# Kernel optimization log

Hardware: AMD Instinct MI355X
Metric: run time of the kernel (lower is better)

Reference implementation:

```python
import jax, jax.numpy as jnp
import numpy as np

N_QUBITS = 8
DEPTH = 2
INPUT_DIM = 64
HIDDEN_DIM = 8
SEQ_LEN = 128
BATCH = 512
DIM = 2 ** N_QUBITS


def _build_perm():
    """Compose the depth*n CNOT ring (CNOT(i,(i+1)%n) for i in range(n), repeated DEPTH times)
    into a single basis-state permutation. Wire 0 is the most-significant qubit (torchquantum order).
    CNOT is an involution on basis states: new[s] = old[f(s)], f flips target bit iff control bit set.
    Sequential composition: perm <- perm[f_j]."""
    n = N_QUBITS
    perm = np.arange(DIM)
    for _ in range(DEPTH):
        for c in range(n):
            t = (c + 1) % n
            s = np.arange(DIM)
            cbit = (s >> (n - 1 - c)) & 1
            fs = np.where(cbit == 1, s ^ (1 << (n - 1 - t)), s)
            perm = perm[fs]
    return jnp.asarray(perm, dtype=jnp.int32)


def _build_signs():
    s = np.arange(DIM)[:, None]
    w = np.arange(N_QUBITS)[None, :]
    bits = (s >> (N_QUBITS - 1 - w)) & 1
    return jnp.asarray(1.0 - 2.0 * bits, dtype=jnp.float32)  # [DIM, n]


PERM = _build_perm()
SIGNS = _build_signs()


def _qlayer(ang):
    """QLayer: RX(ang_i) on wire i of |0...0> (encoder RX + trainable RX fused since RX(a)RX(b)=RX(a+b)),
    then DEPTH CNOT-ring layers (precomputed permutation), then PauliZ expectation per wire.
    ang: [B, n] -> returns [B, n]."""
    half = 0.5 * ang
    v0 = jnp.cos(half).astype(jnp.complex64)          # [B, n]
    v1 = (-1j) * jnp.sin(half).astype(jnp.complex64)  # RX|0> = cos(t/2)|0> - i sin(t/2)|1>
    vecs = jnp.stack([v0, v1], axis=-1)               # [B, n, 2]
    b = ang.shape[0]
    state = jnp.ones((b, 1), jnp.complex64)
    for w in range(N_QUBITS):  # build product state, wire 0 most significant
        state = (state[:, :, None] * vecs[:, w, None, :]).reshape(b, -1)
    state = state[:, PERM]  # apply composed CNOT entanglers
    probs = jnp.real(state * jnp.conj(state)).astype(jnp.float32)  # [B, 2^n]
    return probs @ SIGNS  # [B, n] PauliZ expectations


def setup_inputs() -> dict:
    key = jax.random.key(0)
    ks = jax.random.split(key, 14)
    d = {"inputs": jax.random.normal(ks[0], (SEQ_LEN, BATCH, INPUT_DIM), jnp.float32)}
    fan_in = INPUT_DIM + HIDDEN_DIM
    scale = 1.0 / np.sqrt(fan_in)
    names = ["f", "i", "u", "o"]
    for j, nm in enumerate(names):
        d[f"W_{nm}"] = jax.random.uniform(ks[1 + 3 * j], (N_QUBITS, fan_in), jnp.float32, -scale, scale)
        d[f"b_{nm}"] = jax.random.uniform(ks[2 + 3 * j], (N_QUBITS,), jnp.float32, -scale, scale)
        d[f"th_{nm}"] = jax.random.normal(ks[3 + 3 * j], (N_QUBITS,), jnp.float32) * 0.1
    return d


def reference(inputs, W_f, b_f, W_i, b_i, W_u, b_u, W_o, b_o, th_f, th_i, th_u, th_o):
    batch = inputs.shape[1]

    def step(carry, x):
        hx, cx = carry
        comb = jnp.concatenate([x, hx], axis=1)  # [B, input+hidden]
        f = jax.nn.sigmoid(_qlayer(comb @ W_f.T + b_f + th_f))
        i = jax.nn.sigmoid(_qlayer(comb @ W_i.T + b_i + th_i))
        g = jnp.tanh(_qlayer(comb @ W_u.T + b_u + th_u))
        o = jax.nn.sigmoid(_qlayer(comb @ W_o.T + b_o + th_o))
        cx = f * cx + i * g
        hx = o * jnp.tanh(cx)
        return (hx, cx), hx

    init = (jnp.zeros((batch, HIDDEN_DIM), jnp.float32), jnp.zeros((batch, HIDDEN_DIM), jnp.float32))
    (hx, cx), outputs = jax.lax.scan(step, init, inputs)
    return (outputs, (hx, cx))
```

## Files before the change

### kernel.cpp

```cpp
#include <hip/hip_runtime.h>
#include <cstdint>
#include <cstddef>


constexpr int SEQ    = 128;
constexpr int NBATCH = 512;
constexpr int INDIM  = 64;
constexpr int FANIN  = 72;
constexpr long OUT_HX = (long)SEQ * NBATCH * 8;
constexpr long OUT_CX = OUT_HX + (long)NBATCH * 8;

#define SWZ(v, imm) __int_as_float(__builtin_amdgcn_ds_swizzle(__float_as_int(v), (imm)))

__device__ __forceinline__ float fast_cos(float ang) {
    const float rev = ang * 0.15915494309189535f;
    return __builtin_amdgcn_cosf(__builtin_amdgcn_fractf(rev));
}

template <int CTRL> __device__ __forceinline__ float DPPF(float x) {
    return __int_as_float(__builtin_amdgcn_update_dpp(
        0, __float_as_int(x), CTRL, 0xF, 0xF, false));
}
__device__ __forceinline__ float xlane1(float x) { return DPPF<0xB1>(x); }
__device__ __forceinline__ float xlane2(float x) { return DPPF<0x4E>(x); }
__device__ __forceinline__ float xlane4(float x) { return DPPF<0x141>(DPPF<0x1B>(x)); }
__device__ __forceinline__ float xlane8(float x) { return DPPF<0x128>(x); }

__global__ __launch_bounds__(256) void xproj_kernel(
    const float* __restrict__ x,
    const float* __restrict__ Wf, const float* __restrict__ bf, const float* __restrict__ thf,
    const float* __restrict__ Wi, const float* __restrict__ bi, const float* __restrict__ thi,
    const float* __restrict__ Wu, const float* __restrict__ bu, const float* __restrict__ thu,
    const float* __restrict__ Wo, const float* __restrict__ bo, const float* __restrict__ tho,
    float* __restrict__ xp)
{
    __shared__ float lx[128 * 68];
    __shared__ float lbias[32];
    const int tid = threadIdx.x;
    const long rowBase = (long)blockIdx.x * 128;

    if (tid < 32) {
        const int g = tid >> 3, w = tid & 7;
        const float* bg = (g == 0) ? bf : (g == 1) ? bi : (g == 2) ? bu : bo;
        const float* tg = (g == 0) ? thf : (g == 1) ? thi : (g == 2) ? thu : tho;
        lbias[tid] = bg[w] + tg[w];
    }

    const float4* xin = reinterpret_cast<const float4*>(x + rowBase * INDIM);
#pragma unroll
    for (int i = 0; i < 8; ++i) {
        const int f   = i * 256 + tid;
        const int row = f >> 4;
        const int kq  = f & 15;
        *reinterpret_cast<float4*>(&lx[row * 68 + kq * 4]) = xin[f];
    }
    __syncthreads();

    const int og = tid & 3;
    const int q  = tid >> 2;
    const float* Wg = (og == 0) ? Wf : (og == 1) ? Wi : (og == 2) ? Wu : Wo;

    float acc[2][8];
#pragma unroll
    for (int r = 0; r < 2; ++r)
#pragma unroll
        for (int j = 0; j < 8; ++j) acc[r][j] = 0.f;

#pragma unroll
    for (int k4 = 0; k4 < 16; ++k4) {
        const float4 x0 = *reinterpret_cast<const float4*>(&lx[q * 68 + k4 * 4]);
        const float4 x1 = *reinterpret_cast<const float4*>(&lx[(q + 64) * 68 + k4 * 4]);
#pragma unroll
        for (int j = 0; j < 8; ++j) {
            const float4 wv = *reinterpret_cast<const float4*>(Wg + j * FANIN + k4 * 4);
            acc[0][j] = fmaf(x0.x, wv.x, acc[0][j]);
            acc[0][j] = fmaf(x0.y, wv.y, acc[0][j]);
            acc[0][j] = fmaf(x0.z, wv.z, acc[0][j]);
            acc[0][j] = fmaf(x0.w, wv.w, acc[0][j]);
            acc[1][j] = fmaf(x1.x, wv.x, acc[1][j]);
            acc[1][j] = fmaf(x1.y, wv.y, acc[1][j]);
            acc[1][j] = fmaf(x1.z, wv.z, acc[1][j]);
            acc[1][j] = fmaf(x1.w, wv.w, acc[1][j]);
        }
    }

#pragma unroll
    for (int r = 0; r < 2; ++r) {
        float4 o0, o1;
        o0.x = acc[r][0] + lbias[og * 8 + 0];
        o0.y = acc[r][1] + lbias[og * 8 + 1];
        o0.z = acc[r][2] + lbias[og * 8 + 2];
        o0.w = acc[r][3] + lbias[og * 8 + 3];
        o1.x = acc[r][4] + lbias[og * 8 + 4];
        o1.y = acc[r][5] + lbias[og * 8 + 5];
        o1.z = acc[r][6] + lbias[og * 8 + 6];
        o1.w = acc[r][7] + lbias[og * 8 + 7];
        float* dst = xp + (rowBase + q + 64 * r) * 32 + og * 8;
        reinterpret_cast<float4*>(dst)[0] = o0;
        reinterpret_cast<float4*>(dst)[1] = o1;
    }
}

__global__ __launch_bounds__(256) void qlstm_scan_kernel(
    const float* __restrict__ xp,
    const float* __restrict__ Wf, const float* __restrict__ Wi,
    const float* __restrict__ Wu, const float* __restrict__ Wo,
    float* __restrict__ out)
{
    const int tid  = threadIdx.x;
    const int lane = tid & 31;
    const int row  = (blockIdx.x << 3) + (tid >> 5);
    const int g    = (lane & 1) | ((lane >> 3) & 2);
    const int w    = (lane >> 1) & 7;

    const float* Wg = (g == 0) ? Wf : (g == 1) ? Wi : (g == 2) ? Wu : Wo;

    float whx[8];
#pragma unroll
    for (int d = 0; d < 8; ++d) whx[d] = Wg[w * FANIN + 64 + (w ^ d)];

    const unsigned mask = (unsigned)((0x55AAD5EAF5FAFDABull >> (w * 8)) & 0xFFull);
    bool pm[8];
#pragma unroll
    for (int d = 0; d < 8; ++d) pm[d] = ((mask >> (w ^ d)) & 1u) != 0u;

    const bool  isU  = (g == 2);
    const float ZL   = isU ? -2.0f : -1.0f;
    const float A    = isU ?  2.0f :  1.0f;
    const float B    = isU ? -1.0f :  0.0f;
    const bool  gOdd = (lane & 1) != 0;
    const bool  gHi  = (lane & 16) != 0;

    const int col = g * 8 + w;

    float hh0=0.f,hh1=0.f,hh2=0.f,hh3=0.f,hh4=0.f,hh5=0.f,hh6=0.f,hh7=0.f;
    float cxl = 0.f;

    float xv0 = xp[(long)row * 32 + col];
    float xv1 = xp[((long)NBATCH + row) * 32 + col];

    for (int t = 0; t < SEQ; ++t) {
        float xv2 = 0.f;
        if (t + 2 < SEQ) xv2 = xp[((long)(t + 2) * NBATCH + row) * 32 + col];

        const float d0 = fmaf(hh0, whx[0], fmaf(hh1, whx[1], fmaf(hh2, whx[2], hh3 * whx[3])));
        const float d1 = fmaf(hh4, whx[4], fmaf(hh5, whx[5], fmaf(hh6, whx[6], hh7 * whx[7])));
        const float ang = xv0 + d0 + d1;

        const float c = fast_cos(ang);

        const float cc0 = c;
        const float cc1 = xlane2(cc0);
        const float cc2 = xlane4(cc0);
        const float cc3 = xlane4(cc1);
        const float cc4 = xlane8(cc0);
        const float cc5 = xlane8(cc1);
        const float cc6 = xlane8(cc2);
        const float cc7 = xlane8(cc3);

        const float p0 = pm[0] ? cc0 : 1.0f;
        const float p1 = pm[1] ? cc1 : 1.0f;
        const float p2 = pm[2] ? cc2 : 1.0f;
        const float p3 = pm[3] ? cc3 : 1.0f;
        const float p4 = pm[4] ? cc4 : 1.0f;
        const float p5 = pm[5] ? cc5 : 1.0f;
        const float p6 = pm[6] ? cc6 : 1.0f;
        const float p7 = pm[7] ? cc7 : 1.0f;
        const float z = ((p0 * p1) * (p2 * p3)) * ((p4 * p5) * (p6 * p7));

        const float e   = __expf(z * ZL);
        const float act = fmaf(A, __builtin_amdgcn_rcpf(1.0f + e), B);

        const float a01 = xlane1(act);
        const float ae  = gOdd ? a01 : act;
        const float ao  = gOdd ? act : a01;
        const float be  = SWZ(ae, 0x401F);
        const float bo  = SWZ(ao, 0x401F);
        const float fg  = gHi ? be : ae;
        const float ig  = gHi ? bo : ao;
        const float ug  = gHi ? ae : be;
        const float og  = gHi ? ao : bo;

        const float ncx = fmaf(fg, cxl, ig * ug);
        const float et  = __expf(-2.0f * ncx);
        const float tc  = fmaf(2.0f, __builtin_amdgcn_rcpf(1.0f + et), -1.0f);
        const float nhx = og * tc;
        cxl = ncx;

        if ((lane & 0x11) == 0) out[((long)t * NBATCH + row) * 8 + w] = nhx;

        hh0 = nhx;
        hh1 = xlane2(hh0);
        hh2 = xlane4(hh0);
        hh3 = xlane4(hh1);
        hh4 = xlane8(hh0);
        hh5 = xlane8(hh1);
        hh6 = xlane8(hh2);
        hh7 = xlane8(hh3);

        xv0 = xv1; xv1 = xv2;
    }

    if ((lane & 0x11) == 0) {
        out[OUT_HX + (long)row * 8 + w] = hh0;
        out[OUT_CX + (long)row * 8 + w] = cxl;
    }
}

__global__ __launch_bounds__(256) void qlstm_scan_fused(
    const float* __restrict__ x,
    const float* __restrict__ Wf, const float* __restrict__ bf, const float* __restrict__ thf,
    const float* __restrict__ Wi, const float* __restrict__ bi, const float* __restrict__ thi,
    const float* __restrict__ Wu, const float* __restrict__ bu, const float* __restrict__ thu,
    const float* __restrict__ Wo, const float* __restrict__ bo, const float* __restrict__ tho,
    float* __restrict__ out)
{
    const int tid  = threadIdx.x;
    const int lane = tid & 31;
    const int row  = (blockIdx.x << 3) + (tid >> 5);
    const int g    = lane >> 3;
    const int w    = lane & 7;

    const float* Wg = (g == 0) ? Wf : (g == 1) ? Wi : (g == 2) ? Wu : Wo;
    const float* bg = (g == 0) ? bf : (g == 1) ? bi : (g == 2) ? bu : bo;
    const float* tg = (g == 0) ? thf : (g == 1) ? thi : (g == 2) ? thu : tho;

    float wh0, wh1, wh2, wh3, wh4, wh5, wh6, wh7;
    {
        const float4* p = reinterpret_cast<const float4*>(Wg + w * FANIN + 64);
        const float4 a = p[0], b4 = p[1];
        wh0 = a.x; wh1 = a.y; wh2 = a.z; wh3 = a.w;
        wh4 = b4.x; wh5 = b4.y; wh6 = b4.z; wh7 = b4.w;
    }
    const float bias = bg[w] + tg[w];
    float wx[64];
#pragma unroll
    for (int k4 = 0; k4 < 16; ++k4) {
        const float4 v = reinterpret_cast<const float4*>(Wg + w * FANIN)[k4];
        wx[4*k4+0] = v.x; wx[4*k4+1] = v.y; wx[4*k4+2] = v.z; wx[4*k4+3] = v.w;
    }

    const unsigned mask = (unsigned)((0x55AAD5EAF5FAFDABull >> (w * 8)) & 0xFFull);
    const bool  isU = (g == 2);
    const float ZL  = isU ? -2.0f : -1.0f;
    const float A   = isU ?  2.0f :  1.0f;
    const float B   = isU ? -1.0f :  0.0f;

    float h0=0,h1=0,h2=0,h3=0,h4=0,h5=0,h6=0,h7=0, cxl=0, nhx=0;

    for (int t = 0; t < SEQ; ++t) {
        const float4* xr4 = reinterpret_cast<const float4*>(x + ((long)t * NBATCH + row) * INDIM);
        float acc = bias;
#pragma unroll
        for (int k4 = 0; k4 < 16; ++k4) {
            const float4 v = xr4[k4];
            acc = fmaf(v.x, wx[4*k4+0], acc);
            acc = fmaf(v.y, wx[4*k4+1], acc);
            acc = fmaf(v.z, wx[4*k4+2], acc);
            acc = fmaf(v.w, wx[4*k4+3], acc);
        }
        float ang = acc;
        ang += fmaf(h0, wh0, fmaf(h1, wh1, fmaf(h2, wh2, h3 * wh3)))
             + fmaf(h4, wh4, fmaf(h5, wh5, fmaf(h6, wh6, h7 * wh7)));

        const float c = fast_cos(ang);
        const float cb0 = SWZ(c, 0x018); const float cb1 = SWZ(c, 0x038);
        const float cb2 = SWZ(c, 0x058); const float cb3 = SWZ(c, 0x078);
        const float cb4 = SWZ(c, 0x098); const float cb5 = SWZ(c, 0x0B8);
        const float cb6 = SWZ(c, 0x0D8); const float cb7 = SWZ(c, 0x0F8);

        const float p0 = (mask & 0x01u) ? cb0 : 1.0f;
        const float p1 = (mask & 0x02u) ? cb1 : 1.0f;
        const float p2 = (mask & 0x04u) ? cb2 : 1.0f;
        const float p3 = (mask & 0x08u) ? cb3 : 1.0f;
        const float p4 = (mask & 0x10u) ? cb4 : 1.0f;
        const float p5 = (mask & 0x20u) ? cb5 : 1.0f;
        const float p6 = (mask & 0x40u) ? cb6 : 1.0f;
        const float p7 = (mask & 0x80u) ? cb7 : 1.0f;
        const float z = ((p0*p1)*(p2*p3)) * ((p4*p5)*(p6*p7));

        const float e   = __expf(z * ZL);
        const float act = fmaf(A, __builtin_amdgcn_rcpf(1.0f + e), B);

        const float fg = SWZ(act, 0x007);
        const float ig = SWZ(act, 0x107);
        const float ug = SWZ(act, 0x207);
        const float og = SWZ(act, 0x307);

        const float ncx = fmaf(fg, cxl, ig * ug);
        const float et  = __expf(-2.0f * ncx);
        const float tc  = fmaf(2.0f, __builtin_amdgcn_rcpf(1.0f + et), -1.0f);
        nhx = og * tc;
        cxl = ncx;

        if (lane < 8) out[((long)t * NBATCH + row) * 8 + lane] = nhx;

        h0 = SWZ(nhx, 0x000); h1 = SWZ(nhx, 0x020);
        h2 = SWZ(nhx, 0x040); h3 = SWZ(nhx, 0x060);
        h4 = SWZ(nhx, 0x080); h5 = SWZ(nhx, 0x0A0);
        h6 = SWZ(nhx, 0x0C0); h7 = SWZ(nhx, 0x0E0);
    }

    if (lane < 8) {
        out[OUT_HX + (long)row * 8 + lane] = nhx;
        out[OUT_CX + (long)row * 8 + lane] = cxl;
    }
}

extern "C" void kernel_launch(void* const* d_in, const int* in_sizes, int n_in,
                              void* d_out, int out_size, void* d_ws, size_t ws_size,
                              hipStream_t stream)
{
    const float* x = (const float*)d_in[0];

    const float *Wf, *bf, *thf, *Wi, *bi, *thi, *Wu, *bu, *thu, *Wo, *bo, *tho;
    if (in_sizes[3] == 8) {
        Wf = (const float*)d_in[1];  bf = (const float*)d_in[2];  thf = (const float*)d_in[3];
        Wi = (const float*)d_in[4];  bi = (const float*)d_in[5];  thi = (const float*)d_in[6];
        Wu = (const float*)d_in[7];  bu = (const float*)d_in[8];  thu = (const float*)d_in[9];
        Wo = (const float*)d_in[10]; bo = (const float*)d_in[11]; tho = (const float*)d_in[12];
    } else {
        Wf = (const float*)d_in[1];  bf = (const float*)d_in[2];
        Wi = (const float*)d_in[3];  bi = (const float*)d_in[4];
        Wu = (const float*)d_in[5];  bu = (const float*)d_in[6];
        Wo = (const float*)d_in[7];  bo = (const float*)d_in[8];
        thf = (const float*)d_in[9]; thi = (const float*)d_in[10];
        thu = (const float*)d_in[11]; tho = (const float*)d_in[12];
    }

    float* out = (float*)d_out;
    float* xp  = (float*)d_ws;
    const size_t need = (size_t)SEQ * NBATCH * 32 * sizeof(float);

    if (ws_size >= need) {
        xproj_kernel<<<(SEQ * NBATCH) / 128, 256, 0, stream>>>(
            x, Wf, bf, thf, Wi, bi, thi, Wu, bu, thu, Wo, bo, tho, xp);
        qlstm_scan_kernel<<<NBATCH / 8, 256, 0, stream>>>(
            xp, Wf, Wi, Wu, Wo, out);
    } else {
        qlstm_scan_fused<<<NBATCH / 8, 256, 0, stream>>>(
            x, Wf, bf, thf, Wi, bi, thi, Wu, bu, thu, Wo, bo, tho, out);
    }
}
```

Measured before the change: 163.7 us.

## Remap scan lanes to wave64 with permlane32 swap and chunked xp prefetch

Changes the scan kernel's lane layout to use full 64-lane waves with two batch rows per wave. Gate pairs are split across the two 32-lane halves and exchanged with permlane32_swap instead of ds_swizzle. The cross-lane broadcasts are rebuilt with new DPP row controls, and the xp loads are prefetched in 16-step register chunks so the serial dependency chain avoids per-step load latency. The cost is higher register pressure, and the new DPP patterns have to reproduce the old lane mapping exactly for correctness.

```diff
diff --git a/kernel.cpp b/kernel.cpp
--- a/kernel.cpp
+++ b/kernel.cpp
@@ -21,10 +21,18 @@
     return __int_as_float(__builtin_amdgcn_update_dpp(
         0, __float_as_int(x), CTRL, 0xF, 0xF, false));
 }
-__device__ __forceinline__ float xlane1(float x) { return DPPF<0xB1>(x); }
-__device__ __forceinline__ float xlane2(float x) { return DPPF<0x4E>(x); }
-__device__ __forceinline__ float xlane4(float x) { return DPPF<0x141>(DPPF<0x1B>(x)); }
-__device__ __forceinline__ float xlane8(float x) { return DPPF<0x128>(x); }
+
+__device__ __forceinline__ float xlane32(float x, bool hiHalf) {
+#if __has_builtin(__builtin_amdgcn_permlane32_swap)
+    typedef unsigned uint2v __attribute__((ext_vector_type(2)));
+    uint2v r = __builtin_amdgcn_permlane32_swap(
+        __float_as_uint(x), __float_as_uint(x), false, false);
+    return __uint_as_float(hiHalf ? r[0] : r[1]);
+#else
+    (void)hiHalf;
+    return __shfl_xor(x, 32, 64);
+#endif
+}
 
 __global__ __launch_bounds__(256) void xproj_kernel(
     const float* __restrict__ x,
@@ -108,10 +116,13 @@
     float* __restrict__ out)
 {
     const int tid  = threadIdx.x;
-    const int lane = tid & 31;
-    const int row  = (blockIdx.x << 3) + (tid >> 5);
-    const int g    = (lane & 1) | ((lane >> 3) & 2);
+    const int lane = tid & 63;
+    const int wv   = tid >> 6;
+    const int g1   = (lane >> 5) & 1;
+    const int g    = (lane & 1) | (g1 << 1);
     const int w    = (lane >> 1) & 7;
+    const int rsub = (lane >> 4) & 1;
+    const int row  = (blockIdx.x << 3) + (wv << 1) + rsub;
 
     const float* Wg = (g == 0) ? Wf : (g == 1) ? Wi : (g == 2) ? Wu : Wo;
 
@@ -124,84 +135,85 @@
 #pragma unroll
     for (int d = 0; d < 8; ++d) pm[d] = ((mask >> (w ^ d)) & 1u) != 0u;
 
-    const bool  isU  = (g == 2);
-    const float ZL   = isU ? -2.0f : -1.0f;
-    const float A    = isU ?  2.0f :  1.0f;
-    const float B    = isU ? -1.0f :  0.0f;
-    const bool  gOdd = (lane & 1) != 0;
-    const bool  gHi  = (lane & 16) != 0;
+    const bool  isU   = (g == 2);
+    const float ZL    = isU ? -2.0f : -1.0f;
+    const float A     = isU ?  2.0f :  1.0f;
+    const float B     = isU ? -1.0f :  0.0f;
+    const bool  gOdd  = (lane & 1) != 0;
+    const bool  gHi   = g1 != 0;
+    const bool  doOut = (lane & 0x21) == 0;
 
     const int col = g * 8 + w;
 
     float hh0=0.f,hh1=0.f,hh2=0.f,hh3=0.f,hh4=0.f,hh5=0.f,hh6=0.f,hh7=0.f;
     float cxl = 0.f;
 
-    float xv0 = xp[(long)row * 32 + col];
-    float xv1 = xp[((long)NBATCH + row) * 32 + col];
-
-    for (int t = 0; t < SEQ; ++t) {
-        float xv2 = 0.f;
-        if (t + 2 < SEQ) xv2 = xp[((long)(t + 2) * NBATCH + row) * 32 + col];
-
-        const float d0 = fmaf(hh0, whx[0], fmaf(hh1, whx[1], fmaf(hh2, whx[2], hh3 * whx[3])));
-        const float d1 = fmaf(hh4, whx[4], fmaf(hh5, whx[5], fmaf(hh6, whx[6], hh7 * whx[7])));
-        const float ang = xv0 + d0 + d1;
-
-        const float c = fast_cos(ang);
-
-        const float cc0 = c;
-        const float cc1 = xlane2(cc0);
-        const float cc2 = xlane4(cc0);
-        const float cc3 = xlane4(cc1);
-        const float cc4 = xlane8(cc0);
-        const float cc5 = xlane8(cc1);
-        const float cc6 = xlane8(cc2);
-        const float cc7 = xlane8(cc3);
-
-        const float p0 = pm[0] ? cc0 : 1.0f;
-        const float p1 = pm[1] ? cc1 : 1.0f;
-        const float p2 = pm[2] ? cc2 : 1.0f;
-        const float p3 = pm[3] ? cc3 : 1.0f;
-        const float p4 = pm[4] ? cc4 : 1.0f;
-        const float p5 = pm[5] ? cc5 : 1.0f;
-        const float p6 = pm[6] ? cc6 : 1.0f;
-        const float p7 = pm[7] ? cc7 : 1.0f;
-        const float z = ((p0 * p1) * (p2 * p3)) * ((p4 * p5) * (p6 * p7));
-
-        const float e   = __expf(z * ZL);
-        const float act = fmaf(A, __builtin_amdgcn_rcpf(1.0f + e), B);
-
-        const float a01 = xlane1(act);
-        const float ae  = gOdd ? a01 : act;
-        const float ao  = gOdd ? act : a01;
-        const float be  = SWZ(ae, 0x401F);
-        const float bo  = SWZ(ao, 0x401F);
-        const float fg  = gHi ? be : ae;
-        const float ig  = gHi ? bo : ao;
-        const float ug  = gHi ? ae : be;
-        const float og  = gHi ? ao : bo;
-
-        const float ncx = fmaf(fg, cxl, ig * ug);
-        const float et  = __expf(-2.0f * ncx);
-        const float tc  = fmaf(2.0f, __builtin_amdgcn_rcpf(1.0f + et), -1.0f);
-        const float nhx = og * tc;
-        cxl = ncx;
-
-        if ((lane & 0x11) == 0) out[((long)t * NBATCH + row) * 8 + w] = nhx;
-
-        hh0 = nhx;
-        hh1 = xlane2(hh0);
-        hh2 = xlane4(hh0);
-        hh3 = xlane4(hh1);
-        hh4 = xlane8(hh0);
-        hh5 = xlane8(hh1);
-        hh6 = xlane8(hh2);
-        hh7 = xlane8(hh3);
-
-        xv0 = xv1; xv1 = xv2;
-    }
-
-    if ((lane & 0x11) == 0) {
+#define QSTEP(XV, T) do {                                                      \
+    const float d0_ = fmaf(hh0, whx[0], fmaf(hh1, whx[1], fmaf(hh2, whx[2], hh3 * whx[3]))); \
+    const float d1_ = fmaf(hh4, whx[4], fmaf(hh5, whx[5], fmaf(hh6, whx[6], hh7 * whx[7]))); \
+    const float ang_ = (XV) + d0_ + d1_;                                       \
+    const float c0_ = fast_cos(ang_);                                          \
+    const float c1_ = DPPF<0x4E>(c0_);                                         \
+    const float c2_ = DPPF<0x141>(DPPF<0x1B>(c0_));                            \
+    const float c3_ = DPPF<0x141>(DPPF<0xB1>(c0_));                            \
+    const float c4_ = DPPF<0x128>(c0_);                                        \
+    const float c5_ = DPPF<0x128>(DPPF<0x4E>(c0_));                            \
+    const float c6_ = DPPF<0x140>(DPPF<0x1B>(c0_));                            \
+    const float c7_ = DPPF<0x140>(DPPF<0xB1>(c0_));                            \
+    const float z_ = (((pm[0]?c0_:1.0f)*(pm[1]?c1_:1.0f))                      \
+                    * ((pm[2]?c2_:1.0f)*(pm[3]?c3_:1.0f)))                     \
+                   * (((pm[4]?c4_:1.0f)*(pm[5]?c5_:1.0f))                      \
+                    * ((pm[6]?c6_:1.0f)*(pm[7]?c7_:1.0f)));                    \
+    const float e_   = __expf(z_ * ZL);                                        \
+    const float act_ = fmaf(A, __builtin_amdgcn_rcpf(1.0f + e_), B);           \
+    const float a01_ = DPPF<0xB1>(act_);                                       \
+    const float ae_  = gOdd ? a01_ : act_;                                     \
+    const float ao_  = gOdd ? act_ : a01_;                                     \
+    const float be_  = xlane32(ae_, gHi);                                      \
+    const float bo_  = xlane32(ao_, gHi);                                      \
+    const float fg_  = gHi ? be_ : ae_;                                        \
+    const float ig_  = gHi ? bo_ : ao_;                                        \
+    const float ug_  = gHi ? ae_ : be_;                                        \
+    const float og_  = gHi ? ao_ : bo_;                                        \
+    const float ncx_ = fmaf(fg_, cxl, ig_ * ug_);                              \
+    const float et_  = __expf(-2.0f * ncx_);                                   \
+    const float tc_  = fmaf(2.0f, __builtin_amdgcn_rcpf(1.0f + et_), -1.0f);   \
+    const float nhx_ = og_ * tc_;                                              \
+    cxl = ncx_;                                                                \
+    if (doOut) out[((long)(T) * NBATCH + row) * 8 + w] = nhx_;                 \
+    hh0 = nhx_;                                                                \
+    hh1 = DPPF<0x4E>(nhx_);                                                    \
+    hh2 = DPPF<0x141>(DPPF<0x1B>(nhx_));                                       \
+    hh3 = DPPF<0x141>(DPPF<0xB1>(nhx_));                                       \
+    hh4 = DPPF<0x128>(nhx_);                                                   \
+    hh5 = DPPF<0x128>(DPPF<0x4E>(nhx_));                                       \
+    hh6 = DPPF<0x140>(DPPF<0x1B>(nhx_));                                       \
+    hh7 = DPPF<0x140>(DPPF<0xB1>(nhx_));                                       \
+} while (0)
+
+    float xva[16], xvb[16];
+#pragma unroll
+    for (int j = 0; j < 16; ++j)
+        xva[j] = xp[((long)j * NBATCH + row) * 32 + col];
+
+#pragma unroll 1
+    for (int ck = 0; ck < 8; ++ck) {
+        const int t0 = ck * 16;
+        if (ck < 7) {
+#pragma unroll
+            for (int j = 0; j < 16; ++j)
+                xvb[j] = xp[((long)(t0 + 16 + j) * NBATCH + row) * 32 + col];
+        }
+#pragma unroll
+        for (int j = 0; j < 16; ++j) {
+            QSTEP(xva[j], t0 + j);
+        }
+#pragma unroll
+        for (int j = 0; j < 16; ++j) xva[j] = xvb[j];
+    }
+#undef QSTEP
+
+    if (doOut) {
         out[OUT_HX + (long)row * 8 + w] = hh0;
         out[OUT_CX + (long)row * 8 + w] = cxl;
     }
```

Measured after the change: 148.7 us. 1.1x faster.
